# Kernel tuning notes

Hardware: AMD Instinct MI355X
Metric: run time of the kernel (lower is better)

The kernel has to match this reference:

```python
import jax, jax.numpy as jnp
import numpy as np

OMEGA_ENC = 0.01   # Encoder.omega
OMEGA_K = 0.1      # KernelMLP.omega
N0, E0 = 4096, 16384     # level-0 graph
N1, E1 = 1024, 8192      # level-1 (pooled) graph
F_IN, H, LAT, DIM = 8, 64, 32, 3
F = H + DIM              # conv input features (x || pos)


def _glorot(key, shape):
    s = jnp.sqrt(2.0 / (shape[0] + shape[-1]))
    return (jax.random.normal(key, shape) * s).astype(jnp.float32)


def setup_inputs() -> dict:
    key = jax.random.key(0)
    ks = jax.random.split(key, 24)
    inp = {
        "x": jax.random.normal(ks[0], (N0, F_IN), jnp.float32),
        "pos": jax.random.normal(ks[1], (N0, DIM), jnp.float32),
        "edge_index": jax.random.randint(ks[2], (2, E0), 0, N0),
        "pool_edge_index1": jax.random.randint(ks[3], (2, E1), 0, N1),
        "pool_pos1": jax.random.normal(ks[4], (N1, DIM), jnp.float32),
        "pool_keep_idx0": jnp.sort(jax.random.randint(ks[5], (N1,), 0, N0)),
        "lin0_w": _glorot(ks[6], (F_IN, H)),
        "lin0_b": 0.01 * jax.random.normal(ks[7], (H,), jnp.float32),
        "lin1_w": _glorot(ks[8], (H, LAT)),
        "lin1_b": 0.01 * jax.random.normal(ks[9], (LAT,), jnp.float32),
    }
    k = 10
    for i in range(2):
        inp[f"conv{i}_k_w0"] = _glorot(ks[k], (DIM + 1, H))
        inp[f"conv{i}_k_b0"] = 0.01 * jax.random.normal(ks[k + 1], (H,), jnp.float32)
        inp[f"conv{i}_k_w1"] = _glorot(ks[k + 2], (H, H))
        inp[f"conv{i}_k_b1"] = 0.01 * jax.random.normal(ks[k + 3], (H,), jnp.float32)
        inp[f"conv{i}_k_w2"] = _glorot(ks[k + 4], (H, F))
        inp[f"conv{i}_k_b2"] = 0.01 * jax.random.normal(ks[k + 5], (F,), jnp.float32)
        inp[f"conv{i}_bias"] = jnp.zeros((H,), jnp.float32)  # zeros() init in torch
        k += 6
    return inp


def _with_self_loops(ei, n):
    # add_remaining_self_loops: input edges are assumed self-loop-free
    loops = jnp.arange(n, dtype=ei.dtype)
    return jnp.concatenate([ei, jnp.stack([loops, loops])], axis=1)


def _kernel_conv(xf, ei, pos, n, w0, b0, w1, b1, w2, b2, bias):
    src, dst = ei[0], ei[1]
    rel = pos[dst] - pos[src]                               # [E,3]
    zero = jnp.all(rel == 0.0, axis=1)                      # self loops -> rho=0, nan phi in torch
    rel_s = jnp.where(zero[:, None], 1.0, rel)              # safe values (avoid nan grads)
    rho = jnp.sqrt(jnp.sum(rel_s * rel_s, axis=1))
    theta = jnp.arctan2(rel_s[:, 1], rel_s[:, 0])
    phi = jnp.arcsin(jnp.clip(rel_s[:, 2] / rho, -1.0, 1.0))
    # torch sets theta/phi to 0 where phi is nan (rho==0); rho itself is 0 there
    rho = jnp.where(zero, 0.0, rho)
    theta = jnp.where(zero, 0.0, theta)
    phi = jnp.where(zero, 0.0, phi)
    feats = jnp.stack([rho, theta / jnp.pi, phi / jnp.pi], axis=1)   # [E,3]
    # KernelMLP lin0 on (feats || channel_id), evaluated for all out channels at once
    base = feats @ w0[:DIM] + b0                            # [E,H]
    ch = jnp.arange(H, dtype=xf.dtype)                      # out_channels == H
    h0 = jnp.sin(OMEGA_K * (base[None] + ch[:, None, None] * w0[DIM][None, None]))  # [C,E,H]
    h1 = jnp.sin(OMEGA_K * (jnp.einsum('ceh,hk->cek', h0, w1) + b1))                # [C,E,H]
    x_j = xf[src]                                           # [E,F]
    # msg[e,c] = (lin2(h1[c,e]) * x_j[e]).sum(); lin2 folded into the contraction
    msg = jnp.einsum('ceh,hf,ef->ec', h1, w2, x_j) + (x_j @ b2)[:, None]            # [E,C]
    return jax.ops.segment_sum(msg, dst, num_segments=n) + bias


def reference(x, edge_index, pos, pool_edge_index1, pool_pos1, pool_keep_idx0,
              lin0_w, lin0_b, lin1_w, lin1_b,
              conv0_k_w0, conv0_k_b0, conv0_k_w1, conv0_k_b1, conv0_k_w2, conv0_k_b2, conv0_bias,
              conv1_k_w0, conv1_k_b0, conv1_k_w1, conv1_k_b1, conv1_k_w2, conv1_k_b2, conv1_bias):
    n0 = x.shape[0]
    h = jnp.sin(OMEGA_ENC * (x @ lin0_w + lin0_b))
    ei0 = _with_self_loops(edge_index, n0)
    h = jnp.sin(OMEGA_ENC * _kernel_conv(jnp.concatenate([h, pos], 1), ei0, pos, n0,
                                         conv0_k_w0, conv0_k_b0, conv0_k_w1, conv0_k_b1,
                                         conv0_k_w2, conv0_k_b2, conv0_bias))
    # max_pool_neighbor_x: per-node max over neighbors incl. self (self loops in ei0)
    h = jax.ops.segment_max(h[ei0[0]], ei0[1], num_segments=n0)[pool_keep_idx0]
    n1 = pool_pos1.shape[0]
    ei1 = _with_self_loops(pool_edge_index1, n1)
    h = jnp.sin(OMEGA_ENC * _kernel_conv(jnp.concatenate([h, pool_pos1], 1), ei1, pool_pos1, n1,
                                         conv1_k_w0, conv1_k_b0, conv1_k_w1, conv1_k_b1,
                                         conv1_k_w2, conv1_k_b2, conv1_bias))
    return jnp.sin(OMEGA_ENC * (h @ lin1_w + lin1_b))   # [N1, LAT]
```

## Files before the change

### kernel.cpp

```cpp
#include <hip/hip_runtime.h>
#include <hip/hip_fp16.h>

#define N0C 4096
#define E0C 16384
#define N1C 1024
#define E1C 8192
#define HC 64
#define FINC 8
#define LATC 32
#define FC 67
#define E0T (E0C + N0C)
#define E1T (E1C + N1C)

typedef float f32x4 __attribute__((ext_vector_type(4)));
typedef _Float16 f16x8 __attribute__((ext_vector_type(8)));

__global__ __launch_bounds__(256) void k_prep(
    const float* __restrict__ x, const float* __restrict__ l0w,
    const float* __restrict__ l0b, const float* __restrict__ posp,
    const float* __restrict__ c0w2, const float* __restrict__ c0b2,
    const float* __restrict__ c0w0, const float* __restrict__ c1w0,
    const float* __restrict__ c0w1, const float* __restrict__ c1w1,
    const int* __restrict__ ei0, const int* __restrict__ ei1,
    _Float16* __restrict__ bC0, _Float16* __restrict__ bS0,
    _Float16* __restrict__ bC1, _Float16* __restrict__ bS1,
    _Float16* __restrict__ w1f0, _Float16* __restrict__ w1f1,
    int* __restrict__ cnt, float* __restrict__ tN, float* __restrict__ dN) {
  if (blockIdx.x < 256) {
    __shared__ float w2s[64][69];
    __shared__ float xr[4][64];
    const int tid = threadIdx.x;
    const int wave = __builtin_amdgcn_readfirstlane(tid >> 6), lane = tid & 63;
    for (int idx = tid; idx < HC * FC; idx += 256)
      w2s[idx / FC][idx % FC] = c0w2[idx];
    __syncthreads();
#pragma unroll
    for (int i = 0; i < 4; ++i) {
      const int n = (blockIdx.x * 4 + wave) + i * 1024;
      float a = l0b[lane];
#pragma unroll
      for (int f = 0; f < FINC; ++f) a = fmaf(x[n * FINC + f], l0w[f * HC + lane], a);
      xr[wave][lane] = sinf(0.01f * a);
      __builtin_amdgcn_wave_barrier();
      const float px = posp[n * 3], py = posp[n * 3 + 1], pz = posp[n * 3 + 2];
      float tl = 0.f, ds = 0.f;
#pragma unroll 8
      for (int f = 0; f < HC; ++f) {
        float xv = xr[wave][f];
        tl = fmaf(xv, w2s[lane][f], tl);
        ds = fmaf(xv, c0b2[f], ds);
      }
      tl = fmaf(px, w2s[lane][64], fmaf(py, w2s[lane][65], fmaf(pz, w2s[lane][66], tl)));
      ds = fmaf(px, c0b2[64], fmaf(py, c0b2[65], fmaf(pz, c0b2[66], ds)));
      tN[n * HC + lane] = tl;
      if (lane == 0) dN[n] = ds;
      __builtin_amdgcn_wave_barrier();
    }
  } else {
    int id = (blockIdx.x - 256) * 256 + threadIdx.x;
    if (id < 8192) {
      int lvl = id >> 12, r = id & 4095;
      int fi = r >> 9, lane = (r >> 3) & 63, j = r & 7;
      int nt = fi & 3, ks = fi >> 2;
      int c = nt * 16 + (lane & 15);
      int h = ks * 32 + (lane >> 4) * 8 + j;
      const float* w = lvl ? c1w0 : c0w0;
      float s, cv;
      sincosf(0.1f * (float)c * w[3 * HC + h], &s, &cv);
      (lvl ? bC1 : bC0)[r] = (_Float16)cv;
      (lvl ? bS1 : bS0)[r] = (_Float16)s;
    } else if (id < 16384) {
      int r0 = id - 8192;
      int lvl = r0 >> 12, r = r0 & 4095;
      int fi = r >> 9, lane = (r >> 3) & 63, j = r & 7;
      int ms = fi & 3, ks = fi >> 2;
      int h = ks * 32 + (lane >> 4) * 8 + j;
      int kout = ms * 16 + (lane & 15);
      const float* w = lvl ? c1w1 : c0w1;
      (lvl ? w1f1 : w1f0)[r] = (_Float16)(0.1f * w[h * HC + kout]);
    } else if (id < 16384 + E0T + E1T) {
      int r = id - 16384;
      if (r < E0T) {
        int dst = (r < E0C) ? ei0[E0C + r] : (r - E0C);
        atomicAdd(cnt + dst, 1);
      } else {
        int e = r - E0T;
        int dst = (e < E1C) ? ei1[E1C + e] : (e - E1C);
        atomicAdd(cnt + N0C + dst, 1);
      }
    }
  }
}

__global__ void k_scan(const int* __restrict__ cnt, int* __restrict__ rp0,
                       int* __restrict__ rp1) {
  __shared__ int wsum[16];
  const int b = blockIdx.x;
  const int n = b ? N1C : N0C;
  const int* c = cnt + (b ? N0C : 0);
  int* rp = b ? rp1 : rp0;
  const int tid = threadIdx.x;
  const int lane = tid & 63, wid = tid >> 6;
  const int per = n >> 10;
  int loc[4];
  int sum = 0;
  for (int j = 0; j < per; ++j) { loc[j] = c[tid * per + j]; sum += loc[j]; }
  int xv = sum;
#pragma unroll
  for (int off = 1; off < 64; off <<= 1) {
    int v = __shfl_up(xv, off, 64);
    if (lane >= off) xv += v;
  }
  if (lane == 63) wsum[wid] = xv;
  __syncthreads();
  if (wid == 0) {
    int w = (lane < 16) ? wsum[lane] : 0;
#pragma unroll
    for (int off = 1; off < 16; off <<= 1) {
      int v = __shfl_up(w, off, 64);
      if (lane >= off) w += v;
    }
    if (lane < 16) wsum[lane] = w;
  }
  __syncthreads();
  int prefix = wid ? wsum[wid - 1] : 0;
  int incl = xv + prefix;
  int base = incl - sum;
  for (int j = 0; j < per; ++j) { rp[tid * per + j] = base; base += loc[j]; }
  if (tid == 1023) rp[n] = incl;
}

__global__ void k_scatter(const int* __restrict__ ei0, const int* __restrict__ ei1,
                          const int* __restrict__ rp0, const int* __restrict__ rp1,
                          int* __restrict__ fill, int* __restrict__ eidx0,
                          int* __restrict__ eidx1, int* __restrict__ inv0,
                          int* __restrict__ inv1) {
  int id = blockIdx.x * blockDim.x + threadIdx.x;
  if (id < E0T) {
    int dst = (id < E0C) ? ei0[E0C + id] : (id - E0C);
    int p = rp0[dst] + atomicAdd(fill + dst, 1);
    eidx0[p] = id;
    inv0[id] = p;
  } else if (id < E0T + E1T) {
    int e = id - E0T;
    int dst = (e < E1C) ? ei1[E1C + e] : (e - E1C);
    int p = rp1[dst] + atomicAdd(fill + N0C + dst, 1);
    eidx1[p] = e;
    inv1[e] = p;
  }
}

__global__ __launch_bounds__(256, 2) void k_conv(
    const int* __restrict__ ei, int E, int eTot,
    const float* __restrict__ posp,
    const float* __restrict__ tN, const float* __restrict__ dN,
    const float* __restrict__ kw0, const float* __restrict__ kb0,
    const _Float16* __restrict__ bC, const _Float16* __restrict__ bS,
    const _Float16* __restrict__ w1f, const float* __restrict__ b1,
    const int* __restrict__ inv, float* __restrict__ msg) {
  __shared__ __attribute__((aligned(16))) _Float16 scS[4][2][64], scC[4][2][64];
  const int tid = threadIdx.x;
  const int wave = __builtin_amdgcn_readfirstlane(tid >> 6), lane = tid & 63;
  const int q = lane >> 4;

  f16x8 w1r[8], cbr[8], sbr[8];
#pragma unroll
  for (int f = 0; f < 8; ++f) {
    w1r[f] = *(const f16x8*)(w1f + ((f << 6) + lane) * 8);
    cbr[f] = *(const f16x8*)(bC + ((f << 6) + lane) * 8);
    sbr[f] = *(const f16x8*)(bS + ((f << 6) + lane) * 8);
  }
  f32x4 bbq[4];
#pragma unroll
  for (int ms = 0; ms < 4; ++ms) {
    f32x4 t = *(const f32x4*)(b1 + ms * 16 + q * 4);
    bbq[ms] = t * 0.1f;
  }
  const float kb0v = kb0[lane];
  const float kw0x = kw0[lane], kw0y = kw0[HC + lane], kw0z = kw0[2 * HC + lane];

  const int nW = gridDim.x * 4;
  int e = blockIdx.x * 4 + wave;
  if (e >= eTot) return;

  auto stg = [&](int ee, int& sN, float& sv, float& cv, float& dv) {
    int s, d2;
    if (ee < E) { s = ei[ee]; d2 = ei[E + ee]; } else { s = ee - E; d2 = s; }
    sN = s;
    const float px = posp[s * 3], py = posp[s * 3 + 1], pz = posp[s * 3 + 2];
    const float rx = posp[d2 * 3] - px;
    const float ry = posp[d2 * 3 + 1] - py;
    const float rz = posp[d2 * 3 + 2] - pz;
    float f0 = 0.f, f1 = 0.f, f2 = 0.f;
    if (!(rx == 0.f && ry == 0.f && rz == 0.f)) {
      const float PI_F = 3.14159265358979323846f;
      float rho = sqrtf(rx * rx + ry * ry + rz * rz);
      float th = atan2f(ry, rx);
      float ratio = fminf(1.f, fmaxf(-1.f, rz / rho));
      float ph = asinf(ratio);
      f0 = rho; f1 = th / PI_F; f2 = ph / PI_F;
    }
    float base = fmaf(f0, kw0x, fmaf(f1, kw0y, fmaf(f2, kw0z, kb0v)));
    sincosf(0.1f * base, &sv, &cv);
    dv = dN[s];
  };

  int s0;
  float sv0, cv0, dv0;
  stg(e, s0, sv0, cv0, dv0);
  int buf = 0;
  scS[wave][0][lane] = (_Float16)sv0;
  scC[wave][0][lane] = (_Float16)cv0;
  __builtin_amdgcn_wave_barrier();

  while (true) {
    const int en = e + nW;
    const bool more = en < eTot;
    f32x4 tr[4];
    {
      const float* trp = tN + (size_t)s0 * HC;
#pragma unroll
      for (int ms = 0; ms < 4; ++ms) tr[ms] = *(const f32x4*)(trp + ms * 16 + q * 4);
    }
    const int ip = inv[e];
    int s1 = 0;
    float sv1 = 0.f, cv1 = 0.f, dv1 = 0.f;
    if (more) {
      stg(en, s1, sv1, cv1, dv1);
      scS[wave][buf ^ 1][lane] = (_Float16)sv1;
      scC[wave][buf ^ 1][lane] = (_Float16)cv1;
    }
    __builtin_amdgcn_wave_barrier();

    f32x4 acc[4][4];
#pragma unroll
    for (int ms = 0; ms < 4; ++ms)
#pragma unroll
      for (int nt = 0; nt < 4; ++nt) acc[ms][nt] = bbq[ms];
#pragma unroll
    for (int ks = 0; ks < 2; ++ks) {
      f16x8 sv8 = *(const f16x8*)&scS[wave][buf][ks * 32 + q * 8];
      f16x8 cv8 = *(const f16x8*)&scC[wave][buf][ks * 32 + q * 8];
      f16x8 bf[4];
#pragma unroll
      for (int nt = 0; nt < 4; ++nt)
        bf[nt] = sv8 * cbr[ks * 4 + nt] + cv8 * sbr[ks * 4 + nt];
#pragma unroll
      for (int ms = 0; ms < 4; ++ms)
#pragma unroll
        for (int nt = 0; nt < 4; ++nt)
          acc[ms][nt] = __builtin_amdgcn_mfma_f32_16x16x32_f16(
              w1r[ks * 4 + ms], bf[nt], acc[ms][nt], 0, 0, 0);
    }

    float snt0 = 0.f, snt1 = 0.f, snt2 = 0.f, snt3 = 0.f;
#pragma unroll
    for (int ms = 0; ms < 4; ++ms) {
#pragma unroll
      for (int r = 0; r < 4; ++r) {
        float tt = tr[ms][r];
        snt0 = fmaf(__sinf(acc[ms][0][r]), tt, snt0);
        snt1 = fmaf(__sinf(acc[ms][1][r]), tt, snt1);
        snt2 = fmaf(__sinf(acc[ms][2][r]), tt, snt2);
        snt3 = fmaf(__sinf(acc[ms][3][r]), tt, snt3);
      }
    }
    snt0 += __shfl_xor(snt0, 16, 64); snt0 += __shfl_xor(snt0, 32, 64);
    snt1 += __shfl_xor(snt1, 16, 64); snt1 += __shfl_xor(snt1, 32, 64);
    snt2 += __shfl_xor(snt2, 16, 64); snt2 += __shfl_xor(snt2, 32, 64);
    snt3 += __shfl_xor(snt3, 16, 64); snt3 += __shfl_xor(snt3, 32, 64);
    float val = (q == 0) ? snt0 : (q == 1) ? snt1 : (q == 2) ? snt2 : snt3;
    msg[(size_t)ip * HC + lane] = val + dv0;

    if (!more) break;
    e = en; s0 = s1; dv0 = dv1; buf ^= 1;
  }
}

__global__ void k_reduce0(const float* __restrict__ msg, const int* __restrict__ rp,
                          const float* __restrict__ bias, float* __restrict__ hc) {
  const int wave = threadIdx.x >> 6, lane = threadIdx.x & 63;
  const int n = blockIdx.x * 4 + wave;
  const int j0 = rp[n], j1 = rp[n + 1];
  const float* p = msg + (size_t)j0 * HC + lane;
  const int m = j1 - j0;
  float a0 = 0.f, a1 = 0.f;
  int j = 0;
  for (; j + 1 < m; j += 2) {
    a0 += p[(size_t)j * HC];
    a1 += p[(size_t)(j + 1) * HC];
  }
  if (j < m) a0 += p[(size_t)j * HC];
  hc[(size_t)n * HC + lane] = sinf(0.01f * (a0 + a1 + bias[lane]));
}

__global__ void k_pool1(const float* __restrict__ hc0, const int* __restrict__ eidx,
                        const int* __restrict__ rp, const int* __restrict__ ei,
                        const int* __restrict__ keep, const float* __restrict__ ppos,
                        const float* __restrict__ c1w2, const float* __restrict__ c1b2,
                        float* __restrict__ tN, float* __restrict__ dN) {
  __shared__ float w2s[64][69];
  __shared__ float xr[4][64];
  const int tid = threadIdx.x;
  const int wave = __builtin_amdgcn_readfirstlane(tid >> 6), lane = tid & 63;
  for (int idx = tid; idx < HC * FC; idx += 256)
    w2s[idx / FC][idx % FC] = c1w2[idx];
  const int i = blockIdx.x * 4 + wave;
  int n = keep[i];
  int j0 = rp[n], j1 = rp[n + 1];
  float m = -INFINITY;
  for (int j = j0; j < j1; ++j) {
    int e = eidx[j];
    int src = (e < E0C) ? ei[e] : (e - E0C);
    m = fmaxf(m, hc0[(size_t)src * HC + lane]);
  }
  xr[wave][lane] = m;
  __syncthreads();
  const float px = ppos[i * 3], py = ppos[i * 3 + 1], pz = ppos[i * 3 + 2];
  float tl = 0.f, ds = 0.f;
#pragma unroll 8
  for (int f = 0; f < HC; ++f) {
    float xv = xr[wave][f];
    tl = fmaf(xv, w2s[lane][f], tl);
    ds = fmaf(xv, c1b2[f], ds);
  }
  tl = fmaf(px, w2s[lane][64], fmaf(py, w2s[lane][65], fmaf(pz, w2s[lane][66], tl)));
  ds = fmaf(px, c1b2[64], fmaf(py, c1b2[65], fmaf(pz, c1b2[66], ds)));
  tN[i * HC + lane] = tl;
  if (lane == 0) dN[i] = ds;
}

__global__ void k_reduce1f(const float* __restrict__ msg, const int* __restrict__ rp,
                           const float* __restrict__ bias, const float* __restrict__ l1w,
                           const float* __restrict__ l1b, float* __restrict__ outp) {
  __shared__ float hr[4][64];
  const int wave = threadIdx.x >> 6, lane = threadIdx.x & 63;
  const int node = blockIdx.x * 4 + wave;
  const int j0 = rp[node], j1 = rp[node + 1];
  const float* p = msg + (size_t)j0 * HC + lane;
  const int m = j1 - j0;
  float a0 = 0.f, a1 = 0.f;
  int j = 0;
  for (; j + 1 < m; j += 2) {
    a0 += p[(size_t)j * HC];
    a1 += p[(size_t)(j + 1) * HC];
  }
  if (j < m) a0 += p[(size_t)j * HC];
  hr[wave][lane] = sinf(0.01f * (a0 + a1 + bias[lane]));
  __syncthreads();
  if (lane < LATC) {
    const float* h = hr[wave];
    float o = l1b[lane];
#pragma unroll 8
    for (int c = 0; c < HC; ++c) o = fmaf(h[c], l1w[c * LATC + lane], o);
    outp[node * LATC + lane] = sinf(0.01f * o);
  }
}

extern "C" void kernel_launch(void* const* d_in, const int* in_sizes, int n_in,
                              void* d_out, int out_size, void* d_ws, size_t ws_size,
                              hipStream_t stream) {
  (void)in_sizes; (void)n_in; (void)out_size; (void)ws_size;
  const float* x    = (const float*)d_in[0];
  const float* pos  = (const float*)d_in[1];
  const int*   ei   = (const int*)d_in[2];
  const int*   pei  = (const int*)d_in[3];
  const float* ppos = (const float*)d_in[4];
  const int*   keep = (const int*)d_in[5];
  const float* l0w  = (const float*)d_in[6];
  const float* l0b  = (const float*)d_in[7];
  const float* l1w  = (const float*)d_in[8];
  const float* l1b  = (const float*)d_in[9];
  const float* c0w0 = (const float*)d_in[10];
  const float* c0b0 = (const float*)d_in[11];
  const float* c0w1 = (const float*)d_in[12];
  const float* c0b1 = (const float*)d_in[13];
  const float* c0w2 = (const float*)d_in[14];
  const float* c0b2 = (const float*)d_in[15];
  const float* c0bias = (const float*)d_in[16];
  const float* c1w0 = (const float*)d_in[17];
  const float* c1b0 = (const float*)d_in[18];
  const float* c1w1 = (const float*)d_in[19];
  const float* c1b1 = (const float*)d_in[20];
  const float* c1w2 = (const float*)d_in[21];
  const float* c1b2 = (const float*)d_in[22];
  const float* c1bias = (const float*)d_in[23];
  float* outp = (float*)d_out;

  char* p = (char*)d_ws;
  auto carve = [&](size_t bytes) -> char* {
    char* r = p;
    p += (bytes + 255) & ~(size_t)255;
    return r;
  };
  float* hc0  = (float*)carve((size_t)N0C * HC * 4);
  float* tN0  = (float*)carve((size_t)N0C * HC * 4);
  float* dN0  = (float*)carve((size_t)N0C * 4);
  float* tN1  = (float*)carve((size_t)N1C * HC * 4);
  float* dN1  = (float*)carve((size_t)N1C * 4);
  _Float16* bC0  = (_Float16*)carve(4096 * 2);
  _Float16* bS0  = (_Float16*)carve(4096 * 2);
  _Float16* bC1  = (_Float16*)carve(4096 * 2);
  _Float16* bS1  = (_Float16*)carve(4096 * 2);
  _Float16* w1f0 = (_Float16*)carve(4096 * 2);
  _Float16* w1f1 = (_Float16*)carve(4096 * 2);
  int* cnt  = (int*)carve((size_t)(N0C + N1C) * 4);
  int* fill = (int*)carve((size_t)(N0C + N1C) * 4);
  int* rp0 = (int*)carve((size_t)(N0C + 1) * 4);
  int* rp1 = (int*)carve((size_t)(N1C + 1) * 4);
  int* eidx0 = (int*)carve((size_t)E0T * 4);
  int* eidx1 = (int*)carve((size_t)E1T * 4);
  int* inv0  = (int*)carve((size_t)E0T * 4);
  int* inv1  = (int*)carve((size_t)E1T * 4);
  float* msg = (float*)carve((size_t)E0T * HC * 4);

  hipMemsetAsync(cnt, 0, (size_t)(N0C + N1C) * 4 * 2, stream);

  k_prep<<<256 + 180, 256, 0, stream>>>(x, l0w, l0b, pos, c0w2, c0b2,
                                        c0w0, c1w0, c0w1, c1w1, ei, pei,
                                        bC0, bS0, bC1, bS1, w1f0, w1f1,
                                        cnt, tN0, dN0);
  k_scan<<<2, 1024, 0, stream>>>(cnt, rp0, rp1);
  k_scatter<<<(E0T + E1T + 255) / 256, 256, 0, stream>>>(ei, pei, rp0, rp1, fill,
                                                         eidx0, eidx1, inv0, inv1);
  k_conv<<<512, 256, 0, stream>>>(ei, E0C, E0T, pos, tN0, dN0, c0w0, c0b0,
                                  bC0, bS0, w1f0, c0b1, inv0, msg);
  k_reduce0<<<N0C / 4, 256, 0, stream>>>(msg, rp0, c0bias, hc0);
  k_pool1<<<N1C / 4, 256, 0, stream>>>(hc0, eidx0, rp0, ei, keep, ppos,
                                       c1w2, c1b2, tN1, dN1);
  k_conv<<<512, 256, 0, stream>>>(pei, E1C, E1T, ppos, tN1, dN1, c1w0, c1b0,
                                  bC1, bS1, w1f1, c1b1, inv1, msg);
  k_reduce1f<<<N1C / 4, 256, 0, stream>>>(msg, rp1, c1bias, l1w, l1b, outp);
}
```

Baseline: 182.2 us.

## Fuse all stages into one persistent kernel with atomic grid barriers

Replaces the eight separate kernel launches (prep, scan, scatter, two convs, reductions, pool) with a single persistent kernel of 256 blocks that advances through phases separated by a software grid barrier built on an atomic counter. The goal is to remove per-launch overhead and the idle gaps between dependent kernels. In exchange, the conv phases now run on 256 blocks instead of 512, so fewer waves are available to hide latency. The barrier also relies on every block being resident at once, and the scan now runs on 256 threads per block instead of 1024.

```diff
diff --git a/kernel.cpp b/kernel.cpp
--- a/kernel.cpp
+++ b/kernel.cpp
@@ -11,158 +11,72 @@
 #define FC 67
 #define E0T (E0C + N0C)
 #define E1T (E1C + N1C)
+#define NBLK 256
 
 typedef float f32x4 __attribute__((ext_vector_type(4)));
 typedef _Float16 f16x8 __attribute__((ext_vector_type(8)));
 
-__global__ __launch_bounds__(256) void k_prep(
-    const float* __restrict__ x, const float* __restrict__ l0w,
-    const float* __restrict__ l0b, const float* __restrict__ posp,
-    const float* __restrict__ c0w2, const float* __restrict__ c0b2,
-    const float* __restrict__ c0w0, const float* __restrict__ c1w0,
-    const float* __restrict__ c0w1, const float* __restrict__ c1w1,
-    const int* __restrict__ ei0, const int* __restrict__ ei1,
-    _Float16* __restrict__ bC0, _Float16* __restrict__ bS0,
-    _Float16* __restrict__ bC1, _Float16* __restrict__ bS1,
-    _Float16* __restrict__ w1f0, _Float16* __restrict__ w1f1,
-    int* __restrict__ cnt, float* __restrict__ tN, float* __restrict__ dN) {
-  if (blockIdx.x < 256) {
-    __shared__ float w2s[64][69];
-    __shared__ float xr[4][64];
-    const int tid = threadIdx.x;
-    const int wave = __builtin_amdgcn_readfirstlane(tid >> 6), lane = tid & 63;
-    for (int idx = tid; idx < HC * FC; idx += 256)
-      w2s[idx / FC][idx % FC] = c0w2[idx];
-    __syncthreads();
-#pragma unroll
-    for (int i = 0; i < 4; ++i) {
-      const int n = (blockIdx.x * 4 + wave) + i * 1024;
-      float a = l0b[lane];
-#pragma unroll
-      for (int f = 0; f < FINC; ++f) a = fmaf(x[n * FINC + f], l0w[f * HC + lane], a);
-      xr[wave][lane] = sinf(0.01f * a);
-      __builtin_amdgcn_wave_barrier();
-      const float px = posp[n * 3], py = posp[n * 3 + 1], pz = posp[n * 3 + 2];
-      float tl = 0.f, ds = 0.f;
+struct KArgs {
+  const float *x, *pos;
+  const int *ei, *pei;
+  const float *ppos;
+  const int *keep;
+  const float *l0w, *l0b, *l1w, *l1b;
+  const float *c0w0, *c0b0, *c0w1, *c0b1, *c0w2, *c0b2, *c0bias;
+  const float *c1w0, *c1b0, *c1w1, *c1b1, *c1w2, *c1b2, *c1bias;
+  float *hc0, *tN0, *dN0, *tN1, *dN1;
+  _Float16 *bC0, *bS0, *bC1, *bS1, *w1f0, *w1f1;
+  int *cnt, *fill, *bar, *rp0, *rp1, *eidx0, *eidx1, *inv0, *inv1;
+  float *msg, *outp;
+};
+
+struct SharedPrep { float w2s[64][69]; float xr[4][64]; };
+union SharedU {
+  SharedPrep prep;
+  struct { _Float16 scS[4][2][64]; _Float16 scC[4][2][64]; } conv;
+  struct { int wsum[4]; } scan;
+  struct { float hr[4][64]; } red;
+};
+
+__device__ __forceinline__ void gsync(int* bar, int phase) {
+  __syncthreads();
+  if (threadIdx.x == 0) {
+    __threadfence();
+    __hip_atomic_fetch_add(bar, 1, __ATOMIC_RELEASE, __HIP_MEMORY_SCOPE_AGENT);
+    const int target = phase * NBLK;
+    while (__hip_atomic_load(bar, __ATOMIC_ACQUIRE, __HIP_MEMORY_SCOPE_AGENT) <
+           target) {
+      __builtin_amdgcn_s_sleep(8);
+    }
+  }
+  __syncthreads();
+}
+
+__device__ __forceinline__ void node_td(int lane, int wave,
+    const float (*w2s)[69], const float (*xr)[64], const float* b2,
+    float px, float py, float pz, float* tOut, float* dOut, int idx) {
+  float tl = 0.f, ds = 0.f;
 #pragma unroll 8
-      for (int f = 0; f < HC; ++f) {
-        float xv = xr[wave][f];
-        tl = fmaf(xv, w2s[lane][f], tl);
-        ds = fmaf(xv, c0b2[f], ds);
-      }
-      tl = fmaf(px, w2s[lane][64], fmaf(py, w2s[lane][65], fmaf(pz, w2s[lane][66], tl)));
-      ds = fmaf(px, c0b2[64], fmaf(py, c0b2[65], fmaf(pz, c0b2[66], ds)));
-      tN[n * HC + lane] = tl;
-      if (lane == 0) dN[n] = ds;
-      __builtin_amdgcn_wave_barrier();
-    }
-  } else {
-    int id = (blockIdx.x - 256) * 256 + threadIdx.x;
-    if (id < 8192) {
-      int lvl = id >> 12, r = id & 4095;
-      int fi = r >> 9, lane = (r >> 3) & 63, j = r & 7;
-      int nt = fi & 3, ks = fi >> 2;
-      int c = nt * 16 + (lane & 15);
-      int h = ks * 32 + (lane >> 4) * 8 + j;
-      const float* w = lvl ? c1w0 : c0w0;
-      float s, cv;
-      sincosf(0.1f * (float)c * w[3 * HC + h], &s, &cv);
-      (lvl ? bC1 : bC0)[r] = (_Float16)cv;
-      (lvl ? bS1 : bS0)[r] = (_Float16)s;
-    } else if (id < 16384) {
-      int r0 = id - 8192;
-      int lvl = r0 >> 12, r = r0 & 4095;
-      int fi = r >> 9, lane = (r >> 3) & 63, j = r & 7;
-      int ms = fi & 3, ks = fi >> 2;
-      int h = ks * 32 + (lane >> 4) * 8 + j;
-      int kout = ms * 16 + (lane & 15);
-      const float* w = lvl ? c1w1 : c0w1;
-      (lvl ? w1f1 : w1f0)[r] = (_Float16)(0.1f * w[h * HC + kout]);
-    } else if (id < 16384 + E0T + E1T) {
-      int r = id - 16384;
-      if (r < E0T) {
-        int dst = (r < E0C) ? ei0[E0C + r] : (r - E0C);
-        atomicAdd(cnt + dst, 1);
-      } else {
-        int e = r - E0T;
-        int dst = (e < E1C) ? ei1[E1C + e] : (e - E1C);
-        atomicAdd(cnt + N0C + dst, 1);
-      }
-    }
-  }
+  for (int f = 0; f < HC; ++f) {
+    float xv = xr[wave][f];
+    tl = fmaf(xv, w2s[lane][f], tl);
+    ds = fmaf(xv, b2[f], ds);
+  }
+  tl = fmaf(px, w2s[lane][64], fmaf(py, w2s[lane][65], fmaf(pz, w2s[lane][66], tl)));
+  ds = fmaf(px, b2[64], fmaf(py, b2[65], fmaf(pz, b2[66], ds)));
+  tOut[idx * HC + lane] = tl;
+  if (lane == 0) dOut[idx] = ds;
 }
 
-__global__ void k_scan(const int* __restrict__ cnt, int* __restrict__ rp0,
-                       int* __restrict__ rp1) {
-  __shared__ int wsum[16];
-  const int b = blockIdx.x;
-  const int n = b ? N1C : N0C;
-  const int* c = cnt + (b ? N0C : 0);
-  int* rp = b ? rp1 : rp0;
-  const int tid = threadIdx.x;
-  const int lane = tid & 63, wid = tid >> 6;
-  const int per = n >> 10;
-  int loc[4];
-  int sum = 0;
-  for (int j = 0; j < per; ++j) { loc[j] = c[tid * per + j]; sum += loc[j]; }
-  int xv = sum;
-#pragma unroll
-  for (int off = 1; off < 64; off <<= 1) {
-    int v = __shfl_up(xv, off, 64);
-    if (lane >= off) xv += v;
-  }
-  if (lane == 63) wsum[wid] = xv;
-  __syncthreads();
-  if (wid == 0) {
-    int w = (lane < 16) ? wsum[lane] : 0;
-#pragma unroll
-    for (int off = 1; off < 16; off <<= 1) {
-      int v = __shfl_up(w, off, 64);
-      if (lane >= off) w += v;
-    }
-    if (lane < 16) wsum[lane] = w;
-  }
-  __syncthreads();
-  int prefix = wid ? wsum[wid - 1] : 0;
-  int incl = xv + prefix;
-  int base = incl - sum;
-  for (int j = 0; j < per; ++j) { rp[tid * per + j] = base; base += loc[j]; }
-  if (tid == 1023) rp[n] = incl;
-}
-
-__global__ void k_scatter(const int* __restrict__ ei0, const int* __restrict__ ei1,
-                          const int* __restrict__ rp0, const int* __restrict__ rp1,
-                          int* __restrict__ fill, int* __restrict__ eidx0,
-                          int* __restrict__ eidx1, int* __restrict__ inv0,
-                          int* __restrict__ inv1) {
-  int id = blockIdx.x * blockDim.x + threadIdx.x;
-  if (id < E0T) {
-    int dst = (id < E0C) ? ei0[E0C + id] : (id - E0C);
-    int p = rp0[dst] + atomicAdd(fill + dst, 1);
-    eidx0[p] = id;
-    inv0[id] = p;
-  } else if (id < E0T + E1T) {
-    int e = id - E0T;
-    int dst = (e < E1C) ? ei1[E1C + e] : (e - E1C);
-    int p = rp1[dst] + atomicAdd(fill + N0C + dst, 1);
-    eidx1[p] = e;
-    inv1[e] = p;
-  }
-}
-
-__global__ __launch_bounds__(256, 2) void k_conv(
-    const int* __restrict__ ei, int E, int eTot,
-    const float* __restrict__ posp,
-    const float* __restrict__ tN, const float* __restrict__ dN,
-    const float* __restrict__ kw0, const float* __restrict__ kb0,
-    const _Float16* __restrict__ bC, const _Float16* __restrict__ bS,
-    const _Float16* __restrict__ w1f, const float* __restrict__ b1,
-    const int* __restrict__ inv, float* __restrict__ msg) {
-  __shared__ __attribute__((aligned(16))) _Float16 scS[4][2][64], scC[4][2][64];
-  const int tid = threadIdx.x;
-  const int wave = __builtin_amdgcn_readfirstlane(tid >> 6), lane = tid & 63;
+__device__ __forceinline__ void conv_phase(
+    int waveId, int nWaves, int lane, _Float16* scSw, _Float16* scCw,
+    const int* ei, int E, int eTot, const float* posp,
+    const float* tN, const float* dN,
+    const float* kw0, const float* kb0,
+    const _Float16* bC, const _Float16* bS,
+    const _Float16* w1f, const float* b1,
+    const int* inv, float* msg) {
   const int q = lane >> 4;
-
   f16x8 w1r[8], cbr[8], sbr[8];
 #pragma unroll
   for (int f = 0; f < 8; ++f) {
@@ -179,10 +93,7 @@
   const float kb0v = kb0[lane];
   const float kw0x = kw0[lane], kw0y = kw0[HC + lane], kw0z = kw0[2 * HC + lane];
 
-  const int nW = gridDim.x * 4;
-  int e = blockIdx.x * 4 + wave;
-  if (e >= eTot) return;
-
+  int e = waveId;
   auto stg = [&](int ee, int& sN, float& sv, float& cv, float& dv) {
     int s, d2;
     if (ee < E) { s = ei[ee]; d2 = ei[E + ee]; } else { s = ee - E; d2 = s; }
@@ -209,12 +120,12 @@
   float sv0, cv0, dv0;
   stg(e, s0, sv0, cv0, dv0);
   int buf = 0;
-  scS[wave][0][lane] = (_Float16)sv0;
-  scC[wave][0][lane] = (_Float16)cv0;
+  scSw[lane] = (_Float16)sv0;
+  scCw[lane] = (_Float16)cv0;
   __builtin_amdgcn_wave_barrier();
 
   while (true) {
-    const int en = e + nW;
+    const int en = e + nWaves;
     const bool more = en < eTot;
     f32x4 tr[4];
     {
@@ -227,8 +138,8 @@
     float sv1 = 0.f, cv1 = 0.f, dv1 = 0.f;
     if (more) {
       stg(en, s1, sv1, cv1, dv1);
-      scS[wave][buf ^ 1][lane] = (_Float16)sv1;
-      scC[wave][buf ^ 1][lane] = (_Float16)cv1;
+      scSw[(buf ^ 1) * 64 + lane] = (_Float16)sv1;
+      scCw[(buf ^ 1) * 64 + lane] = (_Float16)cv1;
     }
     __builtin_amdgcn_wave_barrier();
 
@@ -239,8 +150,8 @@
       for (int nt = 0; nt < 4; ++nt) acc[ms][nt] = bbq[ms];
 #pragma unroll
     for (int ks = 0; ks < 2; ++ks) {
-      f16x8 sv8 = *(const f16x8*)&scS[wave][buf][ks * 32 + q * 8];
-      f16x8 cv8 = *(const f16x8*)&scC[wave][buf][ks * 32 + q * 8];
+      f16x8 sv8 = *(const f16x8*)&scSw[buf * 64 + ks * 32 + q * 8];
+      f16x8 cv8 = *(const f16x8*)&scCw[buf * 64 + ks * 32 + q * 8];
       f16x8 bf[4];
 #pragma unroll
       for (int nt = 0; nt < 4; ++nt)
@@ -277,83 +188,175 @@
   }
 }
 
-__global__ void k_reduce0(const float* __restrict__ msg, const int* __restrict__ rp,
-                          const float* __restrict__ bias, float* __restrict__ hc) {
-  const int wave = threadIdx.x >> 6, lane = threadIdx.x & 63;
-  const int n = blockIdx.x * 4 + wave;
-  const int j0 = rp[n], j1 = rp[n + 1];
-  const float* p = msg + (size_t)j0 * HC + lane;
-  const int m = j1 - j0;
-  float a0 = 0.f, a1 = 0.f;
-  int j = 0;
-  for (; j + 1 < m; j += 2) {
-    a0 += p[(size_t)j * HC];
-    a1 += p[(size_t)(j + 1) * HC];
-  }
-  if (j < m) a0 += p[(size_t)j * HC];
-  hc[(size_t)n * HC + lane] = sinf(0.01f * (a0 + a1 + bias[lane]));
-}
-
-__global__ void k_pool1(const float* __restrict__ hc0, const int* __restrict__ eidx,
-                        const int* __restrict__ rp, const int* __restrict__ ei,
-                        const int* __restrict__ keep, const float* __restrict__ ppos,
-                        const float* __restrict__ c1w2, const float* __restrict__ c1b2,
-                        float* __restrict__ tN, float* __restrict__ dN) {
-  __shared__ float w2s[64][69];
-  __shared__ float xr[4][64];
+__global__ __launch_bounds__(256, 2) void k_mega(KArgs a) {
+  __shared__ __attribute__((aligned(16))) SharedU sh;
   const int tid = threadIdx.x;
-  const int wave = __builtin_amdgcn_readfirstlane(tid >> 6), lane = tid & 63;
-  for (int idx = tid; idx < HC * FC; idx += 256)
-    w2s[idx / FC][idx % FC] = c1w2[idx];
-  const int i = blockIdx.x * 4 + wave;
-  int n = keep[i];
-  int j0 = rp[n], j1 = rp[n + 1];
-  float m = -INFINITY;
-  for (int j = j0; j < j1; ++j) {
-    int e = eidx[j];
-    int src = (e < E0C) ? ei[e] : (e - E0C);
-    m = fmaxf(m, hc0[(size_t)src * HC + lane]);
-  }
-  xr[wave][lane] = m;
-  __syncthreads();
-  const float px = ppos[i * 3], py = ppos[i * 3 + 1], pz = ppos[i * 3 + 2];
-  float tl = 0.f, ds = 0.f;
+  const int bid = blockIdx.x;
+  const int wave = __builtin_amdgcn_readfirstlane(tid >> 6);
+  const int lane = tid & 63;
+  const int waveId = bid * 4 + wave;
+  const int gtid = bid * 256 + tid;
+
+  {
+    for (int idx = tid; idx < HC * FC; idx += 256)
+      sh.prep.w2s[idx / FC][idx % FC] = a.c0w2[idx];
+    __syncthreads();
+#pragma unroll
+    for (int i = 0; i < 4; ++i) {
+      const int n = waveId + i * 1024;
+      float v = a.l0b[lane];
+#pragma unroll
+      for (int f = 0; f < FINC; ++f) v = fmaf(a.x[n * FINC + f], a.l0w[f * HC + lane], v);
+      sh.prep.xr[wave][lane] = sinf(0.01f * v);
+      __builtin_amdgcn_wave_barrier();
+      node_td(lane, wave, sh.prep.w2s, sh.prep.xr, a.c0b2,
+              a.pos[n * 3], a.pos[n * 3 + 1], a.pos[n * 3 + 2], a.tN0, a.dN0, n);
+      __builtin_amdgcn_wave_barrier();
+    }
+    if (gtid < 8192) {
+      int lvl = gtid >> 12, r = gtid & 4095;
+      int fi = r >> 9, ln = (r >> 3) & 63, j = r & 7;
+      int nt = fi & 3, ks = fi >> 2;
+      int c = nt * 16 + (ln & 15);
+      int h = ks * 32 + (ln >> 4) * 8 + j;
+      const float* w = lvl ? a.c1w0 : a.c0w0;
+      float s, cv;
+      sincosf(0.1f * (float)c * w[3 * HC + h], &s, &cv);
+      (lvl ? a.bC1 : a.bC0)[r] = (_Float16)cv;
+      (lvl ? a.bS1 : a.bS0)[r] = (_Float16)s;
+    } else if (gtid < 16384) {
+      int r0 = gtid - 8192;
+      int lvl = r0 >> 12, r = r0 & 4095;
+      int fi = r >> 9, ln = (r >> 3) & 63, j = r & 7;
+      int ms = fi & 3, ks = fi >> 2;
+      int h = ks * 32 + (ln >> 4) * 8 + j;
+      int kout = ms * 16 + (ln & 15);
+      const float* w = lvl ? a.c1w1 : a.c0w1;
+      (lvl ? a.w1f1 : a.w1f0)[r] = (_Float16)(0.1f * w[h * HC + kout]);
+    }
+    if (gtid < E0T + E1T) {
+      if (gtid < E0T) {
+        int dst = (gtid < E0C) ? a.ei[E0C + gtid] : (gtid - E0C);
+        atomicAdd(a.cnt + dst, 1);
+      } else {
+        int e = gtid - E0T;
+        int dst = (e < E1C) ? a.pei[E1C + e] : (e - E1C);
+        atomicAdd(a.cnt + N0C + dst, 1);
+      }
+    }
+  }
+  gsync(a.bar, 1);
+
+  if (bid < 2) {
+    const int n = bid ? N1C : N0C;
+    const int per = bid ? 4 : 16;
+    const int* c = a.cnt + (bid ? N0C : 0);
+    int* rp = bid ? a.rp1 : a.rp0;
+    int loc[16];
+    int sum = 0;
+    for (int j = 0; j < per; ++j) { loc[j] = c[tid * per + j]; sum += loc[j]; }
+    int xv = sum;
+#pragma unroll
+    for (int off = 1; off < 64; off <<= 1) {
+      int v = __shfl_up(xv, off, 64);
+      if (lane >= off) xv += v;
+    }
+    if (lane == 63) sh.scan.wsum[wave] = xv;
+    __syncthreads();
+    int pre = 0;
+    for (int k2 = 0; k2 < wave; ++k2) pre += sh.scan.wsum[k2];
+    int incl = xv + pre;
+    int base = incl - sum;
+    for (int j = 0; j < per; ++j) { rp[tid * per + j] = base; base += loc[j]; }
+    if (tid == 255) rp[n] = incl;
+  }
+  gsync(a.bar, 2);
+
+  if (gtid < E0T + E1T) {
+    if (gtid < E0T) {
+      int dst = (gtid < E0C) ? a.ei[E0C + gtid] : (gtid - E0C);
+      int p = a.rp0[dst] + atomicAdd(a.fill + dst, 1);
+      a.eidx0[p] = gtid;
+      a.inv0[gtid] = p;
+    } else {
+      int e = gtid - E0T;
+      int dst = (e < E1C) ? a.pei[E1C + e] : (e - E1C);
+      int p = a.rp1[dst] + atomicAdd(a.fill + N0C + dst, 1);
+      a.eidx1[p] = e;
+      a.inv1[e] = p;
+    }
+  }
+  gsync(a.bar, 3);
+
+  conv_phase(waveId, 1024, lane, &sh.conv.scS[wave][0][0], &sh.conv.scC[wave][0][0],
+             a.ei, E0C, E0T, a.pos, a.tN0, a.dN0, a.c0w0, a.c0b0,
+             a.bC0, a.bS0, a.w1f0, a.c0b1, a.inv0, a.msg);
+  gsync(a.bar, 4);
+
+#pragma unroll
+  for (int i = 0; i < 4; ++i) {
+    const int n = waveId + i * 1024;
+    const int j0 = a.rp0[n], j1 = a.rp0[n + 1];
+    const float* p = a.msg + (size_t)j0 * HC + lane;
+    const int m = j1 - j0;
+    float a0 = 0.f, a1 = 0.f;
+    int j = 0;
+    for (; j + 1 < m; j += 2) {
+      a0 += p[(size_t)j * HC];
+      a1 += p[(size_t)(j + 1) * HC];
+    }
+    if (j < m) a0 += p[(size_t)j * HC];
+    a.hc0[(size_t)n * HC + lane] = sinf(0.01f * (a0 + a1 + a.c0bias[lane]));
+  }
+  gsync(a.bar, 5);
+
+  {
+    for (int idx = tid; idx < HC * FC; idx += 256)
+      sh.prep.w2s[idx / FC][idx % FC] = a.c1w2[idx];
+    __syncthreads();
+    const int i = waveId;
+    int n = a.keep[i];
+    int j0 = a.rp0[n], j1 = a.rp0[n + 1];
+    float m = -INFINITY;
+    for (int j = j0; j < j1; ++j) {
+      int e = a.eidx0[j];
+      int src = (e < E0C) ? a.ei[e] : (e - E0C);
+      m = fmaxf(m, a.hc0[(size_t)src * HC + lane]);
+    }
+    sh.prep.xr[wave][lane] = m;
+    __builtin_amdgcn_wave_barrier();
+    node_td(lane, wave, sh.prep.w2s, sh.prep.xr, a.c1b2,
+            a.ppos[i * 3], a.ppos[i * 3 + 1], a.ppos[i * 3 + 2], a.tN1, a.dN1, i);
+  }
+  gsync(a.bar, 6);
+
+  conv_phase(waveId, 1024, lane, &sh.conv.scS[wave][0][0], &sh.conv.scC[wave][0][0],
+             a.pei, E1C, E1T, a.ppos, a.tN1, a.dN1, a.c1w0, a.c1b0,
+             a.bC1, a.bS1, a.w1f1, a.c1b1, a.inv1, a.msg);
+  gsync(a.bar, 7);
+
+  {
+    const int node = waveId;
+    const int j0 = a.rp1[node], j1 = a.rp1[node + 1];
+    const float* p = a.msg + (size_t)j0 * HC + lane;
+    const int m = j1 - j0;
+    float a0 = 0.f, a1 = 0.f;
+    int j = 0;
+    for (; j + 1 < m; j += 2) {
+      a0 += p[(size_t)j * HC];
+      a1 += p[(size_t)(j + 1) * HC];
+    }
+    if (j < m) a0 += p[(size_t)j * HC];
+    __syncthreads();
+    sh.red.hr[wave][lane] = sinf(0.01f * (a0 + a1 + a.c1bias[lane]));
+    __builtin_amdgcn_wave_barrier();
+    if (lane < LATC) {
+      const float* h = sh.red.hr[wave];
+      float o = a.l1b[lane];
 #pragma unroll 8
-  for (int f = 0; f < HC; ++f) {
-    float xv = xr[wave][f];
-    tl = fmaf(xv, w2s[lane][f], tl);
-    ds = fmaf(xv, c1b2[f], ds);
-  }
-  tl = fmaf(px, w2s[lane][64], fmaf(py, w2s[lane][65], fmaf(pz, w2s[lane][66], tl)));
-  ds = fmaf(px, c1b2[64], fmaf(py, c1b2[65], fmaf(pz, c1b2[66], ds)));
-  tN[i * HC + lane] = tl;
-  if (lane == 0) dN[i] = ds;
-}
-
-__global__ void k_reduce1f(const float* __restrict__ msg, const int* __restrict__ rp,
-                           const float* __restrict__ bias, const float* __restrict__ l1w,
-                           const float* __restrict__ l1b, float* __restrict__ outp) {
-  __shared__ float hr[4][64];
-  const int wave = threadIdx.x >> 6, lane = threadIdx.x & 63;
-  const int node = blockIdx.x * 4 + wave;
-  const int j0 = rp[node], j1 = rp[node + 1];
-  const float* p = msg + (size_t)j0 * HC + lane;
-  const int m = j1 - j0;
-  float a0 = 0.f, a1 = 0.f;
-  int j = 0;
-  for (; j + 1 < m; j += 2) {
-    a0 += p[(size_t)j * HC];
-    a1 += p[(size_t)(j + 1) * HC];
-  }
-  if (j < m) a0 += p[(size_t)j * HC];
-  hr[wave][lane] = sinf(0.01f * (a0 + a1 + bias[lane]));
-  __syncthreads();
-  if (lane < LATC) {
-    const float* h = hr[wave];
-    float o = l1b[lane];
-#pragma unroll 8
-    for (int c = 0; c < HC; ++c) o = fmaf(h[c], l1w[c * LATC + lane], o);
-    outp[node * LATC + lane] = sinf(0.01f * o);
+      for (int c = 0; c < HC; ++c) o = fmaf(h[c], a.l1w[c * LATC + lane], o);
+      a.outp[node * LATC + lane] = sinf(0.01f * o);
+    }
   }
 }
 
@@ -361,31 +364,32 @@
                               void* d_out, int out_size, void* d_ws, size_t ws_size,
                               hipStream_t stream) {
   (void)in_sizes; (void)n_in; (void)out_size; (void)ws_size;
-  const float* x    = (const float*)d_in[0];
-  const float* pos  = (const float*)d_in[1];
-  const int*   ei   = (const int*)d_in[2];
-  const int*   pei  = (const int*)d_in[3];
-  const float* ppos = (const float*)d_in[4];
-  const int*   keep = (const int*)d_in[5];
-  const float* l0w  = (const float*)d_in[6];
-  const float* l0b  = (const float*)d_in[7];
-  const float* l1w  = (const float*)d_in[8];
-  const float* l1b  = (const float*)d_in[9];
-  const float* c0w0 = (const float*)d_in[10];
-  const float* c0b0 = (const float*)d_in[11];
-  const float* c0w1 = (const float*)d_in[12];
-  const float* c0b1 = (const float*)d_in[13];
-  const float* c0w2 = (const float*)d_in[14];
-  const float* c0b2 = (const float*)d_in[15];
-  const float* c0bias = (const float*)d_in[16];
-  const float* c1w0 = (const float*)d_in[17];
-  const float* c1b0 = (const float*)d_in[18];
-  const float* c1w1 = (const float*)d_in[19];
-  const float* c1b1 = (const float*)d_in[20];
-  const float* c1w2 = (const float*)d_in[21];
-  const float* c1b2 = (const float*)d_in[22];
-  const float* c1bias = (const float*)d_in[23];
-  float* outp = (float*)d_out;
+  KArgs a;
+  a.x    = (const float*)d_in[0];
+  a.pos  = (const float*)d_in[1];
+  a.ei   = (const int*)d_in[2];
+  a.pei  = (const int*)d_in[3];
+  a.ppos = (const float*)d_in[4];
+  a.keep = (const int*)d_in[5];
+  a.l0w  = (const float*)d_in[6];
+  a.l0b  = (const float*)d_in[7];
+  a.l1w  = (const float*)d_in[8];
+  a.l1b  = (const float*)d_in[9];
+  a.c0w0 = (const float*)d_in[10];
+  a.c0b0 = (const float*)d_in[11];
+  a.c0w1 = (const float*)d_in[12];
+  a.c0b1 = (const float*)d_in[13];
+  a.c0w2 = (const float*)d_in[14];
+  a.c0b2 = (const float*)d_in[15];
+  a.c0bias = (const float*)d_in[16];
+  a.c1w0 = (const float*)d_in[17];
+  a.c1b0 = (const float*)d_in[18];
+  a.c1w1 = (const float*)d_in[19];
+  a.c1b1 = (const float*)d_in[20];
+  a.c1w2 = (const float*)d_in[21];
+  a.c1b2 = (const float*)d_in[22];
+  a.c1bias = (const float*)d_in[23];
+  a.outp = (float*)d_out;
 
   char* p = (char*)d_ws;
   auto carve = [&](size_t bytes) -> char* {
@@ -393,42 +397,29 @@
     p += (bytes + 255) & ~(size_t)255;
     return r;
   };
-  float* hc0  = (float*)carve((size_t)N0C * HC * 4);
-  float* tN0  = (float*)carve((size_t)N0C * HC * 4);
-  float* dN0  = (float*)carve((size_t)N0C * 4);
-  float* tN1  = (float*)carve((size_t)N1C * HC * 4);
-  float* dN1  = (float*)carve((size_t)N1C * 4);
-  _Float16* bC0  = (_Float16*)carve(4096 * 2);
-  _Float16* bS0  = (_Float16*)carve(4096 * 2);
-  _Float16* bC1  = (_Float16*)carve(4096 * 2);
-  _Float16* bS1  = (_Float16*)carve(4096 * 2);
-  _Float16* w1f0 = (_Float16*)carve(4096 * 2);
-  _Float16* w1f1 = (_Float16*)carve(4096 * 2);
-  int* cnt  = (int*)carve((size_t)(N0C + N1C) * 4);
-  int* fill = (int*)carve((size_t)(N0C + N1C) * 4);
-  int* rp0 = (int*)carve((size_t)(N0C + 1) * 4);
-  int* rp1 = (int*)carve((size_t)(N1C + 1) * 4);
-  int* eidx0 = (int*)carve((size_t)E0T * 4);
-  int* eidx1 = (int*)carve((size_t)E1T * 4);
-  int* inv0  = (int*)carve((size_t)E0T * 4);
-  int* inv1  = (int*)carve((size_t)E1T * 4);
-  float* msg = (float*)carve((size_t)E0T * HC * 4);
-
-  hipMemsetAsync(cnt, 0, (size_t)(N0C + N1C) * 4 * 2, stream);
-
-  k_prep<<<256 + 180, 256, 0, stream>>>(x, l0w, l0b, pos, c0w2, c0b2,
-                                        c0w0, c1w0, c0w1, c1w1, ei, pei,
-                                        bC0, bS0, bC1, bS1, w1f0, w1f1,
-                                        cnt, tN0, dN0);
-  k_scan<<<2, 1024, 0, stream>>>(cnt, rp0, rp1);
-  k_scatter<<<(E0T + E1T + 255) / 256, 256, 0, stream>>>(ei, pei, rp0, rp1, fill,
-                                                         eidx0, eidx1, inv0, inv1);
-  k_conv<<<512, 256, 0, stream>>>(ei, E0C, E0T, pos, tN0, dN0, c0w0, c0b0,
-                                  bC0, bS0, w1f0, c0b1, inv0, msg);
-  k_reduce0<<<N0C / 4, 256, 0, stream>>>(msg, rp0, c0bias, hc0);
-  k_pool1<<<N1C / 4, 256, 0, stream>>>(hc0, eidx0, rp0, ei, keep, ppos,
-                                       c1w2, c1b2, tN1, dN1);
-  k_conv<<<512, 256, 0, stream>>>(pei, E1C, E1T, ppos, tN1, dN1, c1w0, c1b0,
-                                  bC1, bS1, w1f1, c1b1, inv1, msg);
-  k_reduce1f<<<N1C / 4, 256, 0, stream>>>(msg, rp1, c1bias, l1w, l1b, outp);
+  a.hc0  = (float*)carve((size_t)N0C * HC * 4);
+  a.tN0  = (float*)carve((size_t)N0C * HC * 4);
+  a.dN0  = (float*)carve((size_t)N0C * 4);
+  a.tN1  = (float*)carve((size_t)N1C * HC * 4);
+  a.dN1  = (float*)carve((size_t)N1C * 4);
+  a.bC0  = (_Float16*)carve(4096 * 2);
+  a.bS0  = (_Float16*)carve(4096 * 2);
+  a.bC1  = (_Float16*)carve(4096 * 2);
+  a.bS1  = (_Float16*)carve(4096 * 2);
+  a.w1f0 = (_Float16*)carve(4096 * 2);
+  a.w1f1 = (_Float16*)carve(4096 * 2);
+  a.cnt  = (int*)carve((size_t)(N0C + N1C) * 4);
+  a.fill = (int*)carve((size_t)(N0C + N1C) * 4);
+  a.bar  = (int*)carve(256);
+  a.rp0  = (int*)carve((size_t)(N0C + 1) * 4);
+  a.rp1  = (int*)carve((size_t)(N1C + 1) * 4);
+  a.eidx0 = (int*)carve((size_t)E0T * 4);
+  a.eidx1 = (int*)carve((size_t)E1T * 4);
+  a.inv0  = (int*)carve((size_t)E0T * 4);
+  a.inv1  = (int*)carve((size_t)E1T * 4);
+  a.msg   = (float*)carve((size_t)E0T * HC * 4);
+
+  hipMemsetAsync(a.cnt, 0, (size_t)(N0C + N1C) * 4 * 2 + 256, stream);
+
+  k_mega<<<NBLK, 256, 0, stream>>>(a);
 }
```

Measured after the change: 368.9 us. 2.02x slower.
